# Kernel tuning notes

Hardware: AMD Instinct MI355X
Metric: run time of the kernel (lower is better)

## Reference

```python
import jax, jax.numpy as jnp
import numpy as np

IN_CH = 512
OUT_CH = 512
NUM_GROUPS = 32
EPS = 1e-5


def setup_inputs() -> dict:
    key = jax.random.key(0)
    ks = jax.random.split(key, 8)
    N, C, H, W = 4, IN_CH, 64, 64
    s = 0.02
    return {
        "x": jax.random.normal(ks[0], (N, C, H, W), jnp.float32),
        "gn_scale": jnp.ones((C,), jnp.float32),
        "gn_bias": jnp.zeros((C,), jnp.float32),
        "wq": jax.random.normal(ks[1], (OUT_CH, C), jnp.float32) * s,
        "bq": jnp.zeros((OUT_CH,), jnp.float32),
        "wk": jax.random.normal(ks[2], (OUT_CH, C), jnp.float32) * s,
        "bk": jnp.zeros((OUT_CH,), jnp.float32),
        "wv": jax.random.normal(ks[3], (OUT_CH, C), jnp.float32) * s,
        "bv": jnp.zeros((OUT_CH,), jnp.float32),
        "wo": jax.random.normal(ks[4], (OUT_CH, OUT_CH), jnp.float32) * s,
        "bo": jnp.zeros((OUT_CH,), jnp.float32),
    }


def _group_norm(x, scale, bias):
    # x: [N, C, H, W] -> normalize per (group, spatial)
    N, C, H, W = x.shape
    g = x.reshape(N, NUM_GROUPS, C // NUM_GROUPS, H, W)
    mean = jnp.mean(g, axis=(2, 3, 4), keepdims=True)
    var = jnp.var(g, axis=(2, 3, 4), keepdims=True)
    g = (g - mean) * jax.lax.rsqrt(var + EPS)
    h = g.reshape(N, C, H, W)
    return h * scale[None, :, None, None] + bias[None, :, None, None]


def _conv1x1(x, w, b):
    # x: [N, C_in, H, W], w: [C_out, C_in] -> [N, C_out, H, W]
    return jnp.einsum('nchw,dc->ndhw', x, w) + b[None, :, None, None]


def reference(x, gn_scale, gn_bias, wq, bq, wk, bk, wv, bv, wo, bo):
    N, C, H, W = x.shape
    L = H * W
    h = _group_norm(x, gn_scale, gn_bias)
    q = _conv1x1(h, wq, bq).reshape(N, OUT_CH, L)
    k = _conv1x1(h, wk, bk).reshape(N, OUT_CH, L)
    v = _conv1x1(h, wv, bv).reshape(N, OUT_CH, L)
    scores = jnp.einsum('nci,ncj->nij', q, k) * (OUT_CH ** -0.5)  # [N, L, L]
    att = jax.nn.softmax(scores, axis=-1)
    out = jnp.einsum('nij,ncj->nci', att, v).reshape(N, OUT_CH, H, W)
    out = _conv1x1(out, wo, bo)
    return out + x  # skip_proj is Identity since in_ch == out_ch
```

## Files before the change

kernel.cpp:

```cpp
#include <hip/hip_runtime.h>
#include <math.h>

#define NB   4
#define CCH  512
#define LL   4096
#define GRP  32
#define CPG  16
#define CL   (CCH*LL)
#define EPSV 1e-5f
#define QSTR 1024

typedef __bf16 bf16x8 __attribute__((ext_vector_type(8)));
typedef float  f32x4  __attribute__((ext_vector_type(4)));

#define GLOAD_LDS16(g, l) __builtin_amdgcn_global_load_lds( \
    (const __attribute__((address_space(1))) void*)(g),     \
    (__attribute__((address_space(3))) void*)(l), 16, 0, 0)

__device__ __forceinline__ int swz_slot(int row, int q) {
    return 4 * row + (q ^ ((row >> 1) & 3));
}
__device__ __forceinline__ void swz_src(int l, int& jj, int& cc) {
    jj = l >> 2;
    cc = (l & 3) ^ ((l >> 3) & 3);
}

#define DPPF(x, ctrl) __builtin_bit_cast(float, \
    __builtin_amdgcn_update_dpp(0, __builtin_bit_cast(int, (x)), (ctrl), 0xf, 0xf, false))
__device__ __forceinline__ float red_sum16(float x) {
    x += DPPF(x, 0xB1); x += DPPF(x, 0x4E);
    x += DPPF(x, 0x124); x += DPPF(x, 0x128);
    return x;
}

__global__ __launch_bounds__(1024) void gn_stats(const float* __restrict__ x,
                                                 float* __restrict__ stats) {
    int n = blockIdx.x >> 5, g = blockIdx.x & 31;
    size_t base = ((size_t)n * CCH + (size_t)g * CPG) * LL;
    const float4* xp = (const float4*)(x + base);
    const int NV = CPG * LL / 4;
    int tid = threadIdx.x;
    float s1 = 0.f, s2 = 0.f;
    for (int i = tid; i < NV; i += 1024) {
        float4 v = xp[i];
        s1 += v.x + v.y + v.z + v.w;
        s2 += v.x*v.x + v.y*v.y + v.z*v.z + v.w*v.w;
    }
    __shared__ float red[32];
    for (int o = 32; o; o >>= 1) { s1 += __shfl_down(s1, o); s2 += __shfl_down(s2, o); }
    int lane = tid & 63, w = tid >> 6;
    if (!lane) { red[w] = s1; red[16 + w] = s2; }
    __syncthreads();
    if (tid == 0) {
        float a = 0.f, b = 0.f;
        for (int i = 0; i < 16; ++i) { a += red[i]; b += red[16 + i]; }
        const float inv_n = 1.f / (float)(CPG * LL);
        float mean = a * inv_n;
        float var  = b * inv_n - mean * mean;
        stats[blockIdx.x * 2]     = mean;
        stats[blockIdx.x * 2 + 1] = rsqrtf(var + EPSV);
    }
}

__global__ __launch_bounds__(256) void gn_norm_t(const float* __restrict__ x,
    const float* __restrict__ gamma, const float* __restrict__ beta,
    const float* __restrict__ stats, __bf16* __restrict__ Ht) {
    __shared__ float T[64][65];
    int n = blockIdx.z, c0 = blockIdx.y * 64, l0 = blockIdx.x * 64;
    int tid = threadIdx.x;
    int lx = tid & 63, py = tid >> 6;
    const float* xb = x + (size_t)n * CL;
#pragma unroll
    for (int p = 0; p < 16; ++p) {
        int cl = p * 4 + py;
        int c = c0 + cl;
        int g = c >> 4;
        float mean = stats[(n * GRP + g) * 2];
        float rstd = stats[(n * GRP + g) * 2 + 1];
        float sc = gamma[c] * rstd, bi = beta[c] - mean * sc;
        float v = xb[(size_t)c * LL + l0 + lx];
        T[lx][cl] = v * sc + bi;
    }
    __syncthreads();
    __bf16* hb = Ht + (size_t)n * CL;
#pragma unroll
    for (int p = 0; p < 16; ++p) {
        int ll = p * 4 + py;
        hb[(size_t)(l0 + ll) * CCH + c0 + lx] = (__bf16)T[ll][lx];
    }
}

__global__ __launch_bounds__(256) void tobf16_4(
    const float* __restrict__ s0, const float* __restrict__ s1,
    const float* __restrict__ s2, const float* __restrict__ s3,
    __bf16* __restrict__ dst) {
    const float* sp = (blockIdx.y == 0) ? s0 : (blockIdx.y == 1) ? s1
                    : (blockIdx.y == 2) ? s2 : s3;
    int i = (blockIdx.x * 256 + threadIdx.x) * 4;
    float4 v = *(const float4*)(sp + i);
    __bf16* d = dst + (size_t)blockIdx.y * CCH * CCH + i;
    d[0] = (__bf16)v.x; d[1] = (__bf16)v.y; d[2] = (__bf16)v.z; d[3] = (__bf16)v.w;
}

#define BM 128
#define BN 128
#define BK 32

template<int EPI>
__global__ __launch_bounds__(256) void gemm_nt(
    const __bf16* __restrict__ A, const __bf16* __restrict__ B,
    void* __restrict__ Cv, int M, int N, int K,
    long bsA, long bsB, long bsC, long bsR,
    const float* __restrict__ bias, const float* __restrict__ bias2,
    const float* __restrict__ resid)
{
    __shared__ __align__(16) __bf16 As[BM * BK];
    __shared__ __align__(16) __bf16 Bs[BN * BK];
    const int tid = threadIdx.x;
    const int l = tid & 63, w = tid >> 6;
    const int wm = w >> 1, wn = w & 1;
    const int m0 = blockIdx.y * BM, n0 = blockIdx.x * BN;
    A += (long)blockIdx.z * bsA;
    B += (long)blockIdx.z * bsB;

    f32x4 acc[4][4];
#pragma unroll
    for (int i = 0; i < 4; ++i)
#pragma unroll
        for (int j = 0; j < 4; ++j) acc[i][j] = f32x4{0.f, 0.f, 0.f, 0.f};

    int jj, cc; swz_src(l, jj, cc);
    const int slot = swz_slot(l & 15, l >> 4);

    const __bf16* Ag = A + (size_t)(m0 + w * 16 + jj) * K + cc * 8;
    const __bf16* Bg = B + (size_t)(n0 + w * 16 + jj) * K + cc * 8;
    char* AsB = (char*)As + w * 1024;
    char* BsB = (char*)Bs + w * 1024;

    for (int k0 = 0; k0 < K; k0 += BK) {
        GLOAD_LDS16(Ag + k0,                 AsB);
        GLOAD_LDS16(Ag + k0 + (size_t)64*K,  AsB + 4096);
        GLOAD_LDS16(Bg + k0,                 BsB);
        GLOAD_LDS16(Bg + k0 + (size_t)64*K,  BsB + 4096);
        __syncthreads();
        bf16x8 ar[4], br[4];
#pragma unroll
        for (int t = 0; t < 4; ++t) {
            ar[t] = *(const bf16x8*)(As + (wm*64 + t*16) * BK + slot * 8);
            br[t] = *(const bf16x8*)(Bs + (wn*64 + t*16) * BK + slot * 8);
        }
#pragma unroll
        for (int ti = 0; ti < 4; ++ti)
#pragma unroll
            for (int tj = 0; tj < 4; ++tj)
                acc[ti][tj] = __builtin_amdgcn_mfma_f32_16x16x32_bf16(
                    ar[ti], br[tj], acc[ti][tj], 0, 0, 0);
        __syncthreads();
    }

    const long cb = (long)blockIdx.z * bsC;
    const float* bn = (EPI == 5) ? ((n0 < 512) ? bias : (bias2 - 512)) : nullptr;
#pragma unroll
    for (int ti = 0; ti < 4; ++ti) {
#pragma unroll
        for (int r = 0; r < 4; ++r) {
            int m = m0 + wm*64 + ti*16 + (l >> 4)*4 + r;
            float bv = (EPI == 2 || EPI == 4) ? bias[m] : 0.f;
#pragma unroll
            for (int tj = 0; tj < 4; ++tj) {
                int n = n0 + wn*64 + tj*16 + (l & 15);
                float v = acc[ti][tj][r];
                if (EPI == 5) v += bn[n];
                if (EPI == 2 || EPI == 4) v += bv;
                if (EPI == 4) {
                    float rs = resid[(long)blockIdx.z * bsR + (size_t)m * N + n];
                    ((float*)Cv)[cb + (size_t)m * N + n] = v + rs;
                } else {
                    ((__bf16*)Cv)[cb + (size_t)m * N + n] = (__bf16)v;
                }
            }
        }
    }
}

#define PSTR 88

__global__ __launch_bounds__(512, 2) void flash_attn(
    const __bf16* __restrict__ QK, const __bf16* __restrict__ Vb,
    __bf16* __restrict__ Ot)
{
    __shared__ __align__(16) __bf16 Ks[16 * 64 * 32];
    __shared__ float  Sm[64 * 68];
    __shared__ __align__(16) __bf16 Ps[64 * PSTR];
    __shared__ float Lp[64 * 2];

    const int tid = threadIdx.x;
    const int l = tid & 63, w = tid >> 6;
    const int wi = w & 1, jh = (w >> 1) & 1, kh = w >> 2;
    const int g = l >> 4, c = l & 15;
    const int b = (blockIdx.x & 7) >> 1;
    const int qt = ((blockIdx.x >> 3) << 1) | (blockIdx.x & 1);
    const int i0 = qt * 64;
    const size_t bb2 = (size_t)b * LL * QSTR;
    const size_t bb  = (size_t)b * CL;
    const float alpha = 0.044194173824159216f;

    int jj, cc; swz_src(l, jj, cc);
    const int slot = swz_slot(c, g);

    bf16x8 Qf[2][8];
    {
        const __bf16* Qg = QK + bb2 + (size_t)(i0 + wi*32 + c) * QSTR + kh*256 + g*8;
#pragma unroll
        for (int mi = 0; mi < 2; ++mi)
#pragma unroll
            for (int kc = 0; kc < 8; ++kc)
                Qf[mi][kc] = *(const bf16x8*)(Qg + (size_t)mi*16*QSTR + kc*32);
    }

    f32x4 Oacc[4][4];
#pragma unroll
    for (int mi = 0; mi < 4; ++mi)
#pragma unroll
        for (int ni = 0; ni < 4; ++ni) Oacc[mi][ni] = f32x4{0.f, 0.f, 0.f, 0.f};
    float l_r[4] = {0.f, 0.f, 0.f, 0.f};

    const __bf16* Kb = QK + bb2 + 512;
    const __bf16* Vg = Vb + bb;
    const __bf16* Vt = Vg + (size_t)(w*64 + c) * LL + g*8;

    auto stageK = [&](int j0) {
#pragma unroll
        for (int q = 0; q < 2; ++q) {
            int kc = q * 8 + w;
#pragma unroll
            for (int p = 0; p < 4; ++p) {
                const __bf16* src = Kb + (size_t)(j0 + p*16 + jj) * QSTR + kc*32 + cc*8;
                GLOAD_LDS16(src, (char*)Ks + kc*4096 + p*1024);
            }
        }
    };

    auto expst = [&](const f32x4 (&Sx)[2]) {
        const int er0 = wi*32 + (1 - kh)*16 + g*4;
#pragma unroll
        for (int tj = 0; tj < 2; ++tj)
#pragma unroll
            for (int r = 0; r < 4; ++r)
                Sm[(er0 + r)*68 + (jh*2 + tj)*16 + c] = Sx[tj][r];
    };
    auto smx = [&](const f32x4 (&Sown)[2]) {
        const int row0 = wi*32 + kh*16 + g*4;
#pragma unroll
        for (int r = 0; r < 4; ++r) {
            float rs = 0.f;
#pragma unroll
            for (int tj = 0; tj < 2; ++tj) {
                float p = __expf((Sown[tj][r] + Sm[(row0 + r)*68 + (jh*2 + tj)*16 + c]) * alpha);
                rs += p;
                Ps[(row0 + r) * PSTR + (jh*2 + tj)*16 + c] = (__bf16)p;
            }
            l_r[r] += rs;
        }
    };

    stageK(0);
    for (int t = 0; t < 64; ++t) {
        __syncthreads();

        bf16x8 vf[2][4];
#pragma unroll
        for (int jc = 0; jc < 2; ++jc)
#pragma unroll
            for (int ni = 0; ni < 4; ++ni)
                vf[jc][ni] = *(const bf16x8*)(Vt + (size_t)(ni*16) * LL
                                              + t*64 + jc*32);

        f32x4 S[2][2];
#pragma unroll
        for (int mi = 0; mi < 2; ++mi)
#pragma unroll
            for (int tj = 0; tj < 2; ++tj) S[mi][tj] = f32x4{0.f,0.f,0.f,0.f};
        __builtin_amdgcn_s_setprio(1);
#pragma unroll
        for (int kc = 0; kc < 8; ++kc) {
#pragma unroll
            for (int tj = 0; tj < 2; ++tj) {
                bf16x8 kf = *(const bf16x8*)(Ks + (kh*8 + kc)*2048 + (jh*2 + tj)*512 + slot*8);
#pragma unroll
                for (int mi = 0; mi < 2; ++mi)
                    S[mi][tj] = __builtin_amdgcn_mfma_f32_16x16x32_bf16(Qf[mi][kc], kf, S[mi][tj], 0, 0, 0);
            }
        }
        __builtin_amdgcn_s_setprio(0);

        if (kh) expst(S[0]); else expst(S[1]);
        __syncthreads();

        if (kh) smx(S[1]); else smx(S[0]);
        __syncthreads();
        if (t < 63) stageK((t + 1) * 64);

        __builtin_amdgcn_s_setprio(1);
#pragma unroll
        for (int jc = 0; jc < 2; ++jc) {
            bf16x8 pa[4];
#pragma unroll
            for (int mi = 0; mi < 4; ++mi)
                pa[mi] = *(const bf16x8*)(Ps + (mi*16 + c) * PSTR + jc*32 + g*8);
#pragma unroll
            for (int ni = 0; ni < 4; ++ni)
#pragma unroll
                for (int mi = 0; mi < 4; ++mi)
                    Oacc[mi][ni] = __builtin_amdgcn_mfma_f32_16x16x32_bf16(pa[mi], vf[jc][ni], Oacc[mi][ni], 0, 0, 0);
        }
        __builtin_amdgcn_s_setprio(0);
    }

#pragma unroll
    for (int r = 0; r < 4; ++r) {
        float tot = red_sum16(l_r[r]);
        if (c == 0) Lp[(wi*32 + kh*16 + g*4 + r)*2 + jh] = tot;
    }
    __syncthreads();
#pragma unroll
    for (int mi = 0; mi < 4; ++mi) {
#pragma unroll
        for (int r = 0; r < 4; ++r) {
            int row = mi*16 + g*4 + r;
            float inv = 1.f / (Lp[row*2] + Lp[row*2 + 1]);
#pragma unroll
            for (int ni = 0; ni < 4; ++ni) {
                int col = w*64 + ni*16 + c;
                Ot[bb + (size_t)(i0 + row) * CCH + col] = (__bf16)(Oacc[mi][ni][r] * inv);
            }
        }
    }
}

extern "C" void kernel_launch(void* const* d_in, const int* in_sizes, int n_in,
                              void* d_out, int out_size, void* d_ws, size_t ws_size,
                              hipStream_t stream) {
    const float* x   = (const float*)d_in[0];
    const float* gnw = (const float*)d_in[1];
    const float* gnb = (const float*)d_in[2];
    const float* wq  = (const float*)d_in[3];
    const float* bq  = (const float*)d_in[4];
    const float* wk  = (const float*)d_in[5];
    const float* bk  = (const float*)d_in[6];
    const float* wv  = (const float*)d_in[7];
    const float* bv  = (const float*)d_in[8];
    const float* wo  = (const float*)d_in[9];
    const float* bo  = (const float*)d_in[10];
    float* out = (float*)d_out;

    __bf16* wsb = (__bf16*)d_ws;
    const size_t NCL = (size_t)NB * CL;
    __bf16* Ht  = wsb;
    __bf16* QKt = Ht + NCL;
    __bf16* Vb  = QKt + 2 * NCL;
    __bf16* Ot  = Vb + NCL;
    __bf16* Wb  = Ot + NCL;
    float* stats = (float*)(Wb + (size_t)4 * CCH * CCH);
    __bf16* wqkb = Wb;
    __bf16* wvb  = Wb + (size_t)2 * CCH * CCH;
    __bf16* wob  = Wb + (size_t)3 * CCH * CCH;

    tobf16_4<<<dim3(256, 4), 256, 0, stream>>>(wq, wk, wv, wo, Wb);
    gn_stats<<<NB * GRP, 1024, 0, stream>>>(x, stats);
    gn_norm_t<<<dim3(LL / 64, CCH / 64, NB), 256, 0, stream>>>(x, gnw, gnb, stats, Ht);

    gemm_nt<5><<<dim3(1024 / 128, LL / 128, NB), 256, 0, stream>>>(
        Ht, wqkb, QKt, LL, 1024, CCH, CL, 0, (long)LL * 1024, 0, bq, bk, nullptr);
    gemm_nt<2><<<dim3(LL / 128, CCH / 128, NB), 256, 0, stream>>>(
        wvb, Ht, Vb, CCH, LL, CCH, 0, CL, CL, 0, bv, nullptr, nullptr);

    flash_attn<<<dim3(256), 512, 0, stream>>>(QKt, Vb, Ot);

    gemm_nt<4><<<dim3(LL / 128, CCH / 128, NB), 256, 0, stream>>>(
        wob, Ot, (void*)out, CCH, LL, CCH, 0, CL, CL, CL, bo, nullptr, x);
}
```

Baseline: 387.0 us.

## Halve flash-attention query tile to 32 rows and double the grid

The flash attention kernel now processes 32 query rows per block instead of 64. Each wave holds one 16-row Q fragment, half the output accumulators, and a four-way row-sum reduction. The grid doubles to 512 blocks and the launch bound rises to 4, cutting registers and LDS per block so more blocks and waves can be resident per CU to hide latency. In exchange, every K/V tile is loaded and staged twice as often, and each block does fewer MFMAs per LDS access and barrier.

```diff
diff --git a/kernel.cpp b/kernel.cpp
--- a/kernel.cpp
+++ b/kernel.cpp
@@ -185,14 +185,14 @@
 
 #define PSTR 88
 
-__global__ __launch_bounds__(512, 2) void flash_attn(
+__global__ __launch_bounds__(512, 4) void flash_attn(
     const __bf16* __restrict__ QK, const __bf16* __restrict__ Vb,
     __bf16* __restrict__ Ot)
 {
     __shared__ __align__(16) __bf16 Ks[16 * 64 * 32];
-    __shared__ float  Sm[64 * 68];
-    __shared__ __align__(16) __bf16 Ps[64 * PSTR];
-    __shared__ float Lp[64 * 2];
+    __shared__ float  Sm[32 * 68];
+    __shared__ __align__(16) __bf16 Ps[32 * PSTR];
+    __shared__ float Lp[32 * 4];
 
     const int tid = threadIdx.x;
     const int l = tid & 63, w = tid >> 6;
@@ -200,7 +200,7 @@
     const int g = l >> 4, c = l & 15;
     const int b = (blockIdx.x & 7) >> 1;
     const int qt = ((blockIdx.x >> 3) << 1) | (blockIdx.x & 1);
-    const int i0 = qt * 64;
+    const int i0 = qt * 32;
     const size_t bb2 = (size_t)b * LL * QSTR;
     const size_t bb  = (size_t)b * CL;
     const float alpha = 0.044194173824159216f;
@@ -208,19 +208,17 @@
     int jj, cc; swz_src(l, jj, cc);
     const int slot = swz_slot(c, g);
 
-    bf16x8 Qf[2][8];
+    bf16x8 Qf[8];
     {
-        const __bf16* Qg = QK + bb2 + (size_t)(i0 + wi*32 + c) * QSTR + kh*256 + g*8;
-#pragma unroll
-        for (int mi = 0; mi < 2; ++mi)
-#pragma unroll
-            for (int kc = 0; kc < 8; ++kc)
-                Qf[mi][kc] = *(const bf16x8*)(Qg + (size_t)mi*16*QSTR + kc*32);
-    }
-
-    f32x4 Oacc[4][4];
-#pragma unroll
-    for (int mi = 0; mi < 4; ++mi)
+        const __bf16* Qg = QK + bb2 + (size_t)(i0 + wi*16 + c) * QSTR + kh*256 + g*8;
+#pragma unroll
+        for (int kc = 0; kc < 8; ++kc)
+            Qf[kc] = *(const bf16x8*)(Qg + kc*32);
+    }
+
+    f32x4 Oacc[2][4];
+#pragma unroll
+    for (int mi = 0; mi < 2; ++mi)
 #pragma unroll
         for (int ni = 0; ni < 4; ++ni) Oacc[mi][ni] = f32x4{0.f, 0.f, 0.f, 0.f};
     float l_r[4] = {0.f, 0.f, 0.f, 0.f};
@@ -241,26 +239,21 @@
         }
     };
 
-    auto expst = [&](const f32x4 (&Sx)[2]) {
-        const int er0 = wi*32 + (1 - kh)*16 + g*4;
-#pragma unroll
-        for (int tj = 0; tj < 2; ++tj)
-#pragma unroll
-            for (int r = 0; r < 4; ++r)
-                Sm[(er0 + r)*68 + (jh*2 + tj)*16 + c] = Sx[tj][r];
+    const int row0 = wi*16 + g*4;
+    const int colX = (jh*2 + (1 - kh))*16;
+    const int colO = (jh*2 + kh)*16;
+
+    auto expst = [&](const f32x4& Sx) {
+#pragma unroll
+        for (int r = 0; r < 4; ++r)
+            Sm[(row0 + r)*68 + colX + c] = Sx[r];
     };
-    auto smx = [&](const f32x4 (&Sown)[2]) {
-        const int row0 = wi*32 + kh*16 + g*4;
+    auto smx = [&](const f32x4& Sown) {
 #pragma unroll
         for (int r = 0; r < 4; ++r) {
-            float rs = 0.f;
-#pragma unroll
-            for (int tj = 0; tj < 2; ++tj) {
-                float p = __expf((Sown[tj][r] + Sm[(row0 + r)*68 + (jh*2 + tj)*16 + c]) * alpha);
-                rs += p;
-                Ps[(row0 + r) * PSTR + (jh*2 + tj)*16 + c] = (__bf16)p;
-            }
-            l_r[r] += rs;
+            float p = __expf((Sown[r] + Sm[(row0 + r)*68 + colO + c]) * alpha);
+            Ps[(row0 + r) * PSTR + colO + c] = (__bf16)p;
+            l_r[r] += p;
         }
     };
 
@@ -276,42 +269,38 @@
                 vf[jc][ni] = *(const bf16x8*)(Vt + (size_t)(ni*16) * LL
                                               + t*64 + jc*32);
 
-        f32x4 S[2][2];
-#pragma unroll
-        for (int mi = 0; mi < 2; ++mi)
-#pragma unroll
-            for (int tj = 0; tj < 2; ++tj) S[mi][tj] = f32x4{0.f,0.f,0.f,0.f};
+        f32x4 S[2];
+        S[0] = f32x4{0.f,0.f,0.f,0.f};
+        S[1] = f32x4{0.f,0.f,0.f,0.f};
         __builtin_amdgcn_s_setprio(1);
 #pragma unroll
         for (int kc = 0; kc < 8; ++kc) {
 #pragma unroll
             for (int tj = 0; tj < 2; ++tj) {
                 bf16x8 kf = *(const bf16x8*)(Ks + (kh*8 + kc)*2048 + (jh*2 + tj)*512 + slot*8);
+                S[tj] = __builtin_amdgcn_mfma_f32_16x16x32_bf16(Qf[kc], kf, S[tj], 0, 0, 0);
+            }
+        }
+        __builtin_amdgcn_s_setprio(0);
+
+        if (kh) expst(S[0]); else expst(S[1]);
+        __syncthreads();
+
+        if (kh) smx(S[1]); else smx(S[0]);
+        __syncthreads();
+        if (t < 63) stageK((t + 1) * 64);
+
+        __builtin_amdgcn_s_setprio(1);
+#pragma unroll
+        for (int jc = 0; jc < 2; ++jc) {
+            bf16x8 pa[2];
+#pragma unroll
+            for (int mi = 0; mi < 2; ++mi)
+                pa[mi] = *(const bf16x8*)(Ps + (mi*16 + c) * PSTR + jc*32 + g*8);
+#pragma unroll
+            for (int ni = 0; ni < 4; ++ni)
 #pragma unroll
                 for (int mi = 0; mi < 2; ++mi)
-                    S[mi][tj] = __builtin_amdgcn_mfma_f32_16x16x32_bf16(Qf[mi][kc], kf, S[mi][tj], 0, 0, 0);
-            }
-        }
-        __builtin_amdgcn_s_setprio(0);
-
-        if (kh) expst(S[0]); else expst(S[1]);
-        __syncthreads();
-
-        if (kh) smx(S[1]); else smx(S[0]);
-        __syncthreads();
-        if (t < 63) stageK((t + 1) * 64);
-
-        __builtin_amdgcn_s_setprio(1);
-#pragma unroll
-        for (int jc = 0; jc < 2; ++jc) {
-            bf16x8 pa[4];
-#pragma unroll
-            for (int mi = 0; mi < 4; ++mi)
-                pa[mi] = *(const bf16x8*)(Ps + (mi*16 + c) * PSTR + jc*32 + g*8);
-#pragma unroll
-            for (int ni = 0; ni < 4; ++ni)
-#pragma unroll
-                for (int mi = 0; mi < 4; ++mi)
                     Oacc[mi][ni] = __builtin_amdgcn_mfma_f32_16x16x32_bf16(pa[mi], vf[jc][ni], Oacc[mi][ni], 0, 0, 0);
         }
         __builtin_amdgcn_s_setprio(0);
@@ -320,15 +309,15 @@
 #pragma unroll
     for (int r = 0; r < 4; ++r) {
         float tot = red_sum16(l_r[r]);
-        if (c == 0) Lp[(wi*32 + kh*16 + g*4 + r)*2 + jh] = tot;
+        if (c == 0) Lp[(row0 + r)*4 + jh*2 + kh] = tot;
     }
     __syncthreads();
 #pragma unroll
-    for (int mi = 0; mi < 4; ++mi) {
+    for (int mi = 0; mi < 2; ++mi) {
 #pragma unroll
         for (int r = 0; r < 4; ++r) {
             int row = mi*16 + g*4 + r;
-            float inv = 1.f / (Lp[row*2] + Lp[row*2 + 1]);
+            float inv = 1.f / (Lp[row*4] + Lp[row*4+1] + Lp[row*4+2] + Lp[row*4+3]);
 #pragma unroll
             for (int ni = 0; ni < 4; ++ni) {
                 int col = w*64 + ni*16 + c;
@@ -375,7 +364,7 @@
     gemm_nt<2><<<dim3(LL / 128, CCH / 128, NB), 256, 0, stream>>>(
         wvb, Ht, Vb, CCH, LL, CCH, 0, CL, CL, 0, bv, nullptr, nullptr);
 
-    flash_attn<<<dim3(256), 512, 0, stream>>>(QKt, Vb, Ot);
+    flash_attn<<<dim3(512), 512, 0, stream>>>(QKt, Vb, Ot);
 
     gemm_nt<4><<<dim3(LL / 128, CCH / 128, NB), 256, 0, stream>>>(
         wob, Ot, (void*)out, CCH, LL, CCH, 0, CL, CL, CL, bo, nullptr, x);
```

Result: slower. 506.5 us (+30.9%).

## Split QK^T work by query rows instead of head-dim halves to drop score exchange

Applied to the files above, without the earlier changes.

Each wave now computes the full 512-deep dot product for a 16-row by 32-column score block, rather than half the reduction depth over 32 rows. Partial scores no longer have to be exchanged through shared memory, which removes the Sm buffer and one barrier per tile. The cost is a Q fragment that doubles to 16 registers, which raises register pressure. Each K fragment read from LDS now also feeds one MFMA instead of two.

```diff
diff --git a/kernel.cpp b/kernel.cpp
--- a/kernel.cpp
+++ b/kernel.cpp
@@ -190,13 +190,12 @@
     __bf16* __restrict__ Ot)
 {
     __shared__ __align__(16) __bf16 Ks[16 * 64 * 32];
-    __shared__ float  Sm[64 * 68];
     __shared__ __align__(16) __bf16 Ps[64 * PSTR];
     __shared__ float Lp[64 * 2];
 
     const int tid = threadIdx.x;
     const int l = tid & 63, w = tid >> 6;
-    const int wi = w & 1, jh = (w >> 1) & 1, kh = w >> 2;
+    const int qi = w & 3, jh = w >> 2;
     const int g = l >> 4, c = l & 15;
     const int b = (blockIdx.x & 7) >> 1;
     const int qt = ((blockIdx.x >> 3) << 1) | (blockIdx.x & 1);
@@ -208,14 +207,12 @@
     int jj, cc; swz_src(l, jj, cc);
     const int slot = swz_slot(c, g);
 
-    bf16x8 Qf[2][8];
+    bf16x8 Qf[16];
     {
-        const __bf16* Qg = QK + bb2 + (size_t)(i0 + wi*32 + c) * QSTR + kh*256 + g*8;
-#pragma unroll
-        for (int mi = 0; mi < 2; ++mi)
-#pragma unroll
-            for (int kc = 0; kc < 8; ++kc)
-                Qf[mi][kc] = *(const bf16x8*)(Qg + (size_t)mi*16*QSTR + kc*32);
+        const __bf16* Qg = QK + bb2 + (size_t)(i0 + qi*16 + c) * QSTR + g*8;
+#pragma unroll
+        for (int kc = 0; kc < 16; ++kc)
+            Qf[kc] = *(const bf16x8*)(Qg + kc*32);
     }
 
     f32x4 Oacc[4][4];
@@ -241,29 +238,6 @@
         }
     };
 
-    auto expst = [&](const f32x4 (&Sx)[2]) {
-        const int er0 = wi*32 + (1 - kh)*16 + g*4;
-#pragma unroll
-        for (int tj = 0; tj < 2; ++tj)
-#pragma unroll
-            for (int r = 0; r < 4; ++r)
-                Sm[(er0 + r)*68 + (jh*2 + tj)*16 + c] = Sx[tj][r];
-    };
-    auto smx = [&](const f32x4 (&Sown)[2]) {
-        const int row0 = wi*32 + kh*16 + g*4;
-#pragma unroll
-        for (int r = 0; r < 4; ++r) {
-            float rs = 0.f;
-#pragma unroll
-            for (int tj = 0; tj < 2; ++tj) {
-                float p = __expf((Sown[tj][r] + Sm[(row0 + r)*68 + (jh*2 + tj)*16 + c]) * alpha);
-                rs += p;
-                Ps[(row0 + r) * PSTR + (jh*2 + tj)*16 + c] = (__bf16)p;
-            }
-            l_r[r] += rs;
-        }
-    };
-
     stageK(0);
     for (int t = 0; t < 64; ++t) {
         __syncthreads();
@@ -276,29 +250,36 @@
                 vf[jc][ni] = *(const bf16x8*)(Vt + (size_t)(ni*16) * LL
                                               + t*64 + jc*32);
 
-        f32x4 S[2][2];
-#pragma unroll
-        for (int mi = 0; mi < 2; ++mi)
-#pragma unroll
-            for (int tj = 0; tj < 2; ++tj) S[mi][tj] = f32x4{0.f,0.f,0.f,0.f};
+        f32x4 S[2];
+        S[0] = f32x4{0.f,0.f,0.f,0.f};
+        S[1] = f32x4{0.f,0.f,0.f,0.f};
         __builtin_amdgcn_s_setprio(1);
 #pragma unroll
-        for (int kc = 0; kc < 8; ++kc) {
+        for (int kc = 0; kc < 16; ++kc) {
 #pragma unroll
             for (int tj = 0; tj < 2; ++tj) {
-                bf16x8 kf = *(const bf16x8*)(Ks + (kh*8 + kc)*2048 + (jh*2 + tj)*512 + slot*8);
-#pragma unroll
-                for (int mi = 0; mi < 2; ++mi)
-                    S[mi][tj] = __builtin_amdgcn_mfma_f32_16x16x32_bf16(Qf[mi][kc], kf, S[mi][tj], 0, 0, 0);
+                bf16x8 kf = *(const bf16x8*)(Ks + kc*2048 + (jh*2 + tj)*512 + slot*8);
+                S[tj] = __builtin_amdgcn_mfma_f32_16x16x32_bf16(Qf[kc], kf, S[tj], 0, 0, 0);
             }
         }
         __builtin_amdgcn_s_setprio(0);
 
-        if (kh) expst(S[0]); else expst(S[1]);
+        {
+            const int row0 = qi*16 + g*4;
+#pragma unroll
+            for (int r = 0; r < 4; ++r) {
+                float rs = 0.f;
+#pragma unroll
+                for (int tj = 0; tj < 2; ++tj) {
+                    float p = __expf(S[tj][r] * alpha);
+                    rs += p;
+                    Ps[(row0 + r) * PSTR + (jh*2 + tj)*16 + c] = (__bf16)p;
+                }
+                l_r[r] += rs;
+            }
+        }
         __syncthreads();
 
-        if (kh) smx(S[1]); else smx(S[0]);
-        __syncthreads();
         if (t < 63) stageK((t + 1) * 64);
 
         __builtin_amdgcn_s_setprio(1);
@@ -320,7 +301,7 @@
 #pragma unroll
     for (int r = 0; r < 4; ++r) {
         float tot = red_sum16(l_r[r]);
-        if (c == 0) Lp[(wi*32 + kh*16 + g*4 + r)*2 + jh] = tot;
+        if (c == 0) Lp[(qi*16 + g*4 + r)*2 + jh] = tot;
     }
     __syncthreads();
 #pragma unroll
```

New measurement: 388.7 us. No clear change (+0.4%).
